# Kernel tuning notes

Measured on AMD Instinct MI355X. Metric: run time of the kernel, lower is better.

## Reference

```python
import jax, jax.numpy as jnp
import numpy as np

N, E = 50000, 800000
NF, EF, S = 128, 64, 128

def _lin(key, fan_in, fan_out):
    k1, k2 = jax.random.split(key)
    lim = 1.0 / np.sqrt(fan_in)
    W = jax.random.uniform(k1, (fan_in, fan_out), jnp.float32, -lim, lim)
    b = jax.random.uniform(k2, (fan_out,), jnp.float32, -lim, lim)
    return W, b

def setup_inputs() -> dict:
    key = jax.random.key(0)
    ks = jax.random.split(key, 12)
    x = jax.random.normal(ks[0], (N, NF), jnp.float32)
    edge_index = jax.random.randint(ks[1], (2, E), 0, N, jnp.int64)
    edge_attr = jax.random.normal(ks[2], (E, EF), jnp.float32)
    Wn, bn = _lin(ks[3], NF, S)
    We, be = _lin(ks[4], EF, S)
    Wzc, bzc = _lin(ks[5], S, S)   # GCNConv weight/bias (z gate)
    Wzl, bzl = _lin(ks[6], 2 * S, S)
    Wrc, brc = _lin(ks[7], S, S)
    Wrl, brl = _lin(ks[8], 2 * S, S)
    Whc, bhc = _lin(ks[9], S, S)
    Whl, bhl = _lin(ks[10], 2 * S, S)
    Wout, bout = _lin(ks[11], 3 * S, 1)
    return dict(x=x, edge_index=edge_index, edge_attr=edge_attr,
                Wn=Wn, bn=bn, We=We, be=be,
                Wzc=Wzc, bzc=bzc, Wzl=Wzl, bzl=bzl,
                Wrc=Wrc, brc=brc, Wrl=Wrl, brl=brl,
                Whc=Whc, bhc=bhc, Whl=Whl, bhl=bhl,
                Wout=Wout, bout=bout)

def reference(x, edge_index, edge_attr, Wn, bn, We, be,
              Wzc, bzc, Wzl, bzl, Wrc, brc, Wrl, brl,
              Whc, bhc, Whl, bhl, Wout, bout):
    n = x.shape[0]
    src, dst = edge_index[0], edge_index[1]
    xe = jax.nn.relu(x @ Wn + bn)                      # [N,S]
    ea = jax.nn.relu(edge_attr @ We + be)              # [E,S]
    # GCNConv normalization with self-loops (shared across the 3 gates)
    loop = jnp.arange(n)
    s2 = jnp.concatenate([src, loop])
    d2 = jnp.concatenate([dst, loop])
    deg = jax.ops.segment_sum(jnp.ones(s2.shape[0], xe.dtype), d2, n)
    dinv = jax.lax.rsqrt(deg)                          # deg >= 1 (self loops)
    norm = (dinv[s2] * dinv[d2])[:, None]              # [E+N,1]
    def gcn(W, b):
        xw = xe @ W
        return jax.ops.segment_sum(xw[s2] * norm, d2, n) + b
    H = jnp.zeros_like(xe)
    Z = jax.nn.sigmoid(jnp.concatenate([gcn(Wzc, bzc), H], 1) @ Wzl + bzl)
    R = jax.nn.sigmoid(jnp.concatenate([gcn(Wrc, brc), H], 1) @ Wrl + brl)
    Ht = jnp.tanh(jnp.concatenate([gcn(Whc, bhc), H * R], 1) @ Whl + bhl)
    H = Z * H + (1.0 - Z) * Ht                          # [N,S]
    edge_h = jnp.concatenate([H[src], H[dst], ea], axis=1)  # [E,3S]
    return edge_h @ Wout + bout                         # [E,1]
```

## Files before the change

kernel.cpp:

```cpp
#include <hip/hip_runtime.h>
#include <hip/hip_bf16.h>
#include <math.h>

#define NN 50000
#define EE 800000

typedef __bf16 bf16x8 __attribute__((ext_vector_type(8)));
typedef float f32x4 __attribute__((ext_vector_type(4)));
typedef unsigned int u32x4 __attribute__((ext_vector_type(4)));

__global__ void k_deg_wprep(const int* __restrict__ ei, int* __restrict__ deg,
                            const float* __restrict__ Wzc, const float* __restrict__ bzc,
                            const float* __restrict__ Wzl, const float* __restrict__ bzl,
                            const float* __restrict__ Whc, const float* __restrict__ bhc,
                            const float* __restrict__ Whl, const float* __restrict__ bhl,
                            float* __restrict__ Wcat, float* __restrict__ cb) {
    if (blockIdx.x < 128) {
        int i = blockIdx.x;
        int k = threadIdx.x;
        if (k < 128) {
            float sz = 0.f, sh = 0.f;
            for (int j = 0; j < 128; j++) {
                sz += Wzc[i * 128 + j] * Wzl[j * 128 + k];
                sh += Whc[i * 128 + j] * Whl[j * 128 + k];
            }
            Wcat[i * 256 + 2 * k]     = sz;
            Wcat[i * 256 + 2 * k + 1] = sh;
            if (i == 0) {
                float bz = bzl[k], bh = bhl[k];
                for (int j = 0; j < 128; j++) {
                    bz += bzc[j] * Wzl[j * 128 + k];
                    bh += bhc[j] * Whl[j * 128 + k];
                }
                cb[2 * k]     = bz;
                cb[2 * k + 1] = bh;
            }
        }
    } else {
        int e = (blockIdx.x - 128) * 256 + threadIdx.x;
        if (e < EE) atomicAdd(&deg[ei[EE + e]], 1);
    }
}

__global__ __launch_bounds__(256) void k_g1_mfma(const float* __restrict__ x,
                                                 const float* __restrict__ Wn,
                                                 const float* __restrict__ bn,
                                                 const int* __restrict__ deg,
                                                 __hip_bfloat16* __restrict__ xs) {
    const int lane = threadIdx.x & 63;
    const int ln = lane & 15;
    const int q  = lane >> 4;
    const int wid = (blockIdx.x * 256 + threadIdx.x) >> 6;
    const int nw  = gridDim.x * 4;
    const int ch  = wid & 1;
    const int step = nw >> 1;

    bf16x8 bfrag[4][4];
#pragma unroll
    for (int t = 0; t < 4; t++)
#pragma unroll
        for (int kc = 0; kc < 4; kc++)
#pragma unroll
            for (int j = 0; j < 8; j++)
                bfrag[t][kc][j] = (__bf16)Wn[(kc * 32 + q * 8 + j) * 128 + ch * 64 + t * 16 + ln];
    float biasR[4];
#pragma unroll
    for (int t = 0; t < 4; t++) biasR[t] = bn[ch * 64 + t * 16 + ln];

    for (int rt = wid >> 1; rt < 3125; rt += step) {
        const int e0 = rt * 16;
        const float* arow = x + (size_t)(e0 + ln) * 128;
        bf16x8 af[4];
#pragma unroll
        for (int kc = 0; kc < 4; kc++) {
            float4 v0 = *(const float4*)(arow + kc * 32 + q * 8);
            float4 v1 = *(const float4*)(arow + kc * 32 + q * 8 + 4);
            af[kc][0] = (__bf16)v0.x; af[kc][1] = (__bf16)v0.y;
            af[kc][2] = (__bf16)v0.z; af[kc][3] = (__bf16)v0.w;
            af[kc][4] = (__bf16)v1.x; af[kc][5] = (__bf16)v1.y;
            af[kc][6] = (__bf16)v1.z; af[kc][7] = (__bf16)v1.w;
        }
        f32x4 acc[4];
#pragma unroll
        for (int t = 0; t < 4; t++) acc[t] = (f32x4){0.f, 0.f, 0.f, 0.f};
#pragma unroll
        for (int t = 0; t < 4; t++)
#pragma unroll
            for (int kc = 0; kc < 4; kc++)
                acc[t] = __builtin_amdgcn_mfma_f32_16x16x32_bf16(af[kc], bfrag[t][kc], acc[t], 0, 0, 0);

        float diR[4];
#pragma unroll
        for (int r = 0; r < 4; r++) diR[r] = rsqrtf((float)(deg[e0 + q * 4 + r] + 1));
#pragma unroll
        for (int t = 0; t < 4; t++)
#pragma unroll
            for (int r = 0; r < 4; r++) {
                float v = fmaxf(acc[t][r] + biasR[t], 0.f) * diR[r];
                xs[(size_t)(e0 + q * 4 + r) * 128 + ch * 64 + t * 16 + ln] = __float2bfloat16(v);
            }
    }
}

__global__ void k_scan_a(const int* __restrict__ deg, int* __restrict__ partial) {
    __shared__ int s[256];
    int i = blockIdx.x * 256 + threadIdx.x;
    s[threadIdx.x] = (i < NN) ? deg[i] : 0;
    __syncthreads();
    for (int off = 128; off > 0; off >>= 1) {
        if (threadIdx.x < off) s[threadIdx.x] += s[threadIdx.x + off];
        __syncthreads();
    }
    if (threadIdx.x == 0) partial[blockIdx.x] = s[0];
}

__global__ void k_scan_c(const int* __restrict__ deg, const int* __restrict__ partial,
                         int* __restrict__ rowptr, int* __restrict__ cursor) {
    __shared__ int s[256];
    __shared__ int ps[256];
    int i = blockIdx.x * 256 + threadIdx.x;
    int v = (i < NN) ? deg[i] : 0;
    s[threadIdx.x] = v;
    ps[threadIdx.x] = (threadIdx.x < blockIdx.x) ? partial[threadIdx.x] : 0;
    __syncthreads();
    for (int off = 128; off > 0; off >>= 1) {
        if (threadIdx.x < off) ps[threadIdx.x] += ps[threadIdx.x + off];
        __syncthreads();
    }
    for (int off = 1; off < 256; off <<= 1) {
        int t = (threadIdx.x >= off) ? s[threadIdx.x - off] : 0;
        __syncthreads();
        s[threadIdx.x] += t;
        __syncthreads();
    }
    int excl = s[threadIdx.x] - v + ps[0];
    if (i < NN) { rowptr[i] = excl; cursor[i] = excl; }
    if (i == 0) rowptr[NN] = EE;
}

__global__ void k_fill(const int* __restrict__ ei, int* __restrict__ cursor,
                       int* __restrict__ col) {
    int e = blockIdx.x * 256 + threadIdx.x;
    if (e < EE) {
        int d = ei[EE + e];
        int p = atomicAdd(&cursor[d], 1);
        col[p] = ei[e];
    }
}

__global__ __launch_bounds__(256) void k_gather(const unsigned int* __restrict__ xsu,
                                                const int* __restrict__ rowptr,
                                                const int* __restrict__ col,
                                                const int* __restrict__ deg,
                                                unsigned int* __restrict__ aggu) {
    int gt = blockIdx.x * 256 + threadIdx.x;
    int node = gt >> 6;
    int lane = threadIdx.x & 63;
    if (node >= NN) return;
    const int g = lane >> 4;
    const int k = lane & 15;
    int beg = rowptr[node], end = rowptr[node + 1];

    float acc[8];
#pragma unroll
    for (int i = 0; i < 8; i++) acc[i] = 0.f;

    {
        u32x4 sv = *(const u32x4*)(xsu + (size_t)node * 64 + k * 4);
        if (g == 0) {
#pragma unroll
            for (int d = 0; d < 4; d++) {
                acc[2 * d]     += __uint_as_float(sv[d] << 16);
                acc[2 * d + 1] += __uint_as_float(sv[d] & 0xFFFF0000u);
            }
        }
    }

    int p = beg;
    while (p < end) {
        int rem = end - p;
        int chunk = rem < 64 ? rem : 64;
        int cv = (lane < chunk) ? col[p + lane] : 0;
        for (int j = 0; j < chunk; j += 4) {
            int s = __shfl(cv, j + g);
            u32x4 v = *(const u32x4*)(xsu + (size_t)s * 64 + k * 4);
            if (j + g >= chunk) v = (u32x4){0u, 0u, 0u, 0u};
#pragma unroll
            for (int d = 0; d < 4; d++) {
                acc[2 * d]     += __uint_as_float(v[d] << 16);
                acc[2 * d + 1] += __uint_as_float(v[d] & 0xFFFF0000u);
            }
        }
        p += 64;
    }

#pragma unroll
    for (int off = 16; off < 64; off <<= 1)
#pragma unroll
        for (int i = 0; i < 8; i++) acc[i] += __shfl_xor(acc[i], off);

    float di = rsqrtf((float)(deg[node] + 1));
    unsigned int o0, o1, o2, o3;
    {
        __hip_bfloat16 lo, hi;
        lo = __float2bfloat16(acc[0] * di); hi = __float2bfloat16(acc[1] * di);
        o0 = (unsigned int)*(unsigned short*)&lo | ((unsigned int)*(unsigned short*)&hi << 16);
        lo = __float2bfloat16(acc[2] * di); hi = __float2bfloat16(acc[3] * di);
        o1 = (unsigned int)*(unsigned short*)&lo | ((unsigned int)*(unsigned short*)&hi << 16);
        lo = __float2bfloat16(acc[4] * di); hi = __float2bfloat16(acc[5] * di);
        o2 = (unsigned int)*(unsigned short*)&lo | ((unsigned int)*(unsigned short*)&hi << 16);
        lo = __float2bfloat16(acc[6] * di); hi = __float2bfloat16(acc[7] * di);
        o3 = (unsigned int)*(unsigned short*)&lo | ((unsigned int)*(unsigned short*)&hi << 16);
    }
    int src = lane >> 2;
    unsigned int t0 = __shfl((int)o0, src);
    unsigned int t1 = __shfl((int)o1, src);
    unsigned int t2 = __shfl((int)o2, src);
    unsigned int t3 = __shfl((int)o3, src);
    int c2 = lane & 3;
    unsigned int res = (c2 == 0) ? t0 : (c2 == 1) ? t1 : (c2 == 2) ? t2 : t3;
    aggu[(size_t)node * 64 + lane] = res;
}

__global__ __launch_bounds__(256) void k_gate_red(const unsigned int* __restrict__ aggu,
                                                  const float* __restrict__ Wcat,
                                                  const float* __restrict__ cb,
                                                  const float* __restrict__ Wout,
                                                  float* __restrict__ aArr,
                                                  float* __restrict__ bArr) {
    __shared__ float red[4][32];
    const int lane = threadIdx.x & 63;
    const int ln = lane & 15;
    const int q  = lane >> 4;
    const int w  = threadIdx.x >> 6;

    bf16x8 bfrag[4][4];
#pragma unroll
    for (int t = 0; t < 4; t++)
#pragma unroll
        for (int kc = 0; kc < 4; kc++)
#pragma unroll
            for (int j = 0; j < 8; j++)
                bfrag[t][kc][j] = (__bf16)Wcat[(kc * 32 + q * 8 + j) * 256 + w * 64 + t * 16 + ln];

    float cbR[4], wAR[4], wBR[4];
#pragma unroll
    for (int t = 0; t < 4; t++) {
        int c = w * 64 + t * 16 + ln;
        cbR[t] = cb[c];
        int k = c >> 1;
        wAR[t] = Wout[k];
        wBR[t] = Wout[128 + k];
    }
    const bool odd = (ln & 1);

    for (int rt = blockIdx.x; rt < 3125; rt += gridDim.x) {
        const int e0 = rt * 16;
        const u32x4* arow = (const u32x4*)aggu + (size_t)(e0 + ln) * 16;
        bf16x8 af[4];
#pragma unroll
        for (int kc = 0; kc < 4; kc++) {
            u32x4 uv = arow[kc * 4 + q];
            af[kc] = __builtin_bit_cast(bf16x8, uv);
        }
        f32x4 acc[4];
#pragma unroll
        for (int t = 0; t < 4; t++) acc[t] = (f32x4){0.f, 0.f, 0.f, 0.f};
#pragma unroll
        for (int t = 0; t < 4; t++)
#pragma unroll
            for (int kc = 0; kc < 4; kc++)
                acc[t] = __builtin_amdgcn_mfma_f32_16x16x32_bf16(af[kc], bfrag[t][kc], acc[t], 0, 0, 0);

        float pa[4] = {0.f, 0.f, 0.f, 0.f};
        float pb[4] = {0.f, 0.f, 0.f, 0.f};
#pragma unroll
        for (int t = 0; t < 4; t++)
#pragma unroll
            for (int r = 0; r < 4; r++) {
                float val = acc[t][r] + cbR[t];
                float s = odd ? tanhf(val) : (1.f / (1.f + expf(-val)));
                float partner = __shfl_xor(s, 1);
                if (!odd) {
                    float h = (1.f - s) * partner;
                    pa[r] += h * wAR[t];
                    pb[r] += h * wBR[t];
                }
            }
#pragma unroll
        for (int off = 1; off < 16; off <<= 1) {
#pragma unroll
            for (int r = 0; r < 4; r++) {
                pa[r] += __shfl_xor(pa[r], off);
                pb[r] += __shfl_xor(pb[r], off);
            }
        }
        if (ln < 4) {
            float v = (ln == 0) ? pa[0] : (ln == 1) ? pa[1] : (ln == 2) ? pa[2] : pa[3];
            red[w][q * 4 + ln] = v;
        } else if (ln < 8) {
            int r = ln - 4;
            float v = (r == 0) ? pb[0] : (r == 1) ? pb[1] : (r == 2) ? pb[2] : pb[3];
            red[w][16 + q * 4 + r] = v;
        }
        __syncthreads();
        if (threadIdx.x < 32) {
            int row = threadIdx.x & 15;
            int ab = threadIdx.x >> 4;
            float s = red[0][ab * 16 + row] + red[1][ab * 16 + row]
                    + red[2][ab * 16 + row] + red[3][ab * 16 + row];
            if (ab) bArr[e0 + row] = s; else aArr[e0 + row] = s;
        }
        __syncthreads();
    }
}

__global__ __launch_bounds__(256) void k_edge_mfma(const float* __restrict__ EA,
                                                   const int* __restrict__ ei,
                                                   const float* __restrict__ We,
                                                   const float* __restrict__ be,
                                                   const float* __restrict__ Wout,
                                                   const float* __restrict__ boutp,
                                                   const float* __restrict__ aArr,
                                                   const float* __restrict__ bArr,
                                                   float* __restrict__ out) {
    const int lane = threadIdx.x & 63;
    const int ln = lane & 15;
    const int q  = lane >> 4;
    const int wid = (blockIdx.x * 256 + threadIdx.x) >> 6;
    const int nw  = gridDim.x * 4;

    bf16x8 bfrag[2][8];
#pragma unroll
    for (int h = 0; h < 2; h++)
#pragma unroll
        for (int t = 0; t < 8; t++)
#pragma unroll
            for (int j = 0; j < 8; j++)
                bfrag[h][t][j] = (__bf16)We[(h * 32 + q * 8 + j) * 128 + t * 16 + ln];

    float beR[8], w3R[8];
#pragma unroll
    for (int t = 0; t < 8; t++) {
        beR[t] = be[t * 16 + ln];
        w3R[t] = Wout[256 + t * 16 + ln];
    }
    const float b0 = boutp[0];

    for (int tile = wid; tile < EE / 16; tile += nw) {
        const int e0 = tile * 16;
        const float* arow = EA + (size_t)(e0 + ln) * 64;
        float4 v0 = *(const float4*)(arow + q * 8);
        float4 v1 = *(const float4*)(arow + q * 8 + 4);
        float4 v2 = *(const float4*)(arow + 32 + q * 8);
        float4 v3 = *(const float4*)(arow + 32 + q * 8 + 4);
        bf16x8 af0, af1;
        af0[0] = (__bf16)v0.x; af0[1] = (__bf16)v0.y; af0[2] = (__bf16)v0.z; af0[3] = (__bf16)v0.w;
        af0[4] = (__bf16)v1.x; af0[5] = (__bf16)v1.y; af0[6] = (__bf16)v1.z; af0[7] = (__bf16)v1.w;
        af1[0] = (__bf16)v2.x; af1[1] = (__bf16)v2.y; af1[2] = (__bf16)v2.z; af1[3] = (__bf16)v2.w;
        af1[4] = (__bf16)v3.x; af1[5] = (__bf16)v3.y; af1[6] = (__bf16)v3.z; af1[7] = (__bf16)v3.w;

        f32x4 acc[8];
#pragma unroll
        for (int t = 0; t < 8; t++) acc[t] = (f32x4){0.f, 0.f, 0.f, 0.f};
#pragma unroll
        for (int t = 0; t < 8; t++)
            acc[t] = __builtin_amdgcn_mfma_f32_16x16x32_bf16(af0, bfrag[0][t], acc[t], 0, 0, 0);
#pragma unroll
        for (int t = 0; t < 8; t++)
            acc[t] = __builtin_amdgcn_mfma_f32_16x16x32_bf16(af1, bfrag[1][t], acc[t], 0, 0, 0);

        float part[4] = {0.f, 0.f, 0.f, 0.f};
#pragma unroll
        for (int t = 0; t < 8; t++)
#pragma unroll
            for (int r = 0; r < 4; r++) {
                float y = acc[t][r] + beR[t];
                y = fmaxf(y, 0.f);
                part[r] += y * w3R[t];
            }
#pragma unroll
        for (int off = 1; off < 16; off <<= 1) {
#pragma unroll
            for (int r = 0; r < 4; r++) part[r] += __shfl_xor(part[r], off);
        }
        if (ln < 4) {
            float c = (ln == 0) ? part[0] : (ln == 1) ? part[1] : (ln == 2) ? part[2] : part[3];
            int e = e0 + q * 4 + ln;
            out[e] = c + aArr[ei[e]] + bArr[ei[EE + e]] + b0;
        }
    }
}

extern "C" void kernel_launch(void* const* d_in, const int* in_sizes, int n_in,
                              void* d_out, int out_size, void* d_ws, size_t ws_size,
                              hipStream_t stream) {
    const float* x    = (const float*)d_in[0];
    const int*   ei   = (const int*)d_in[1];
    const float* ea   = (const float*)d_in[2];
    const float* Wn   = (const float*)d_in[3];
    const float* bn   = (const float*)d_in[4];
    const float* We   = (const float*)d_in[5];
    const float* be   = (const float*)d_in[6];
    const float* Wzc  = (const float*)d_in[7];
    const float* bzc  = (const float*)d_in[8];
    const float* Wzl  = (const float*)d_in[9];
    const float* bzl  = (const float*)d_in[10];
    const float* Whc  = (const float*)d_in[15];
    const float* bhc  = (const float*)d_in[16];
    const float* Whl  = (const float*)d_in[17];
    const float* bhl  = (const float*)d_in[18];
    const float* Wout = (const float*)d_in[19];
    const float* bout = (const float*)d_in[20];
    float* out = (float*)d_out;

    char* w = (char*)d_ws;
    auto carve = [&](size_t bytes) {
        void* p = (void*)w;
        w += (bytes + 255) / 256 * 256;
        return p;
    };
    int*   deg     = (int*)carve((size_t)NN * 4);
    float* aArr    = (float*)carve((size_t)NN * 4);
    float* bArr    = (float*)carve((size_t)NN * 4);
    __hip_bfloat16* xs = (__hip_bfloat16*)carve((size_t)NN * 128 * 2);
    unsigned int* aggu = (unsigned int*)carve((size_t)NN * 64 * 4);
    float* Wcat    = (float*)carve(128 * 256 * 4);
    float* cb      = (float*)carve(256 * 4);
    int*   rowptr  = (int*)carve((size_t)(NN + 1) * 4);
    int*   cursor  = (int*)carve((size_t)NN * 4);
    int*   col     = (int*)carve((size_t)EE * 4);
    int*   partial = (int*)carve(256 * 4);

    hipMemsetAsync(deg, 0, (size_t)NN * 4, stream);

    k_deg_wprep<<<128 + 3125, 256, 0, stream>>>(ei, deg, Wzc, bzc, Wzl, bzl,
                                                Whc, bhc, Whl, bhl, Wcat, cb);

    k_g1_mfma<<<384, 256, 0, stream>>>(x, Wn, bn, deg, xs);

    const int NB = (NN + 255) / 256;
    k_scan_a<<<NB, 256, 0, stream>>>(deg, partial);
    k_scan_c<<<NB, 256, 0, stream>>>(deg, partial, rowptr, cursor);
    k_fill<<<3125, 256, 0, stream>>>(ei, cursor, col);

    k_gather<<<(NN * 64 + 255) / 256, 256, 0, stream>>>((const unsigned int*)xs, rowptr, col, deg, aggu);

    k_gate_red<<<512, 256, 0, stream>>>(aggu, Wcat, cb, Wout, aArr, bArr);

    k_edge_mfma<<<2048, 256, 0, stream>>>(ea, ei, We, be, Wout, bout, aArr, bArr, out);
}
```

Measured before the change: 530.0 us.

## Fuse node GEMM into degree kernel and apply source dinv during gather

The node-embedding MFMA GEMM no longer depends on degrees, so it moves into the same launch as the degree-count and weight-prep kernel, with its grid doubled to 768 blocks. The source-side normalization is now applied in the gather by loading a precomputed dinv per neighbor, and dinv is computed once in the scan kernel. This removes one kernel launch and the serial dependency, letting the dense GEMM overlap with the atomic degree counting. In exchange, the gather does an extra scalar load per neighbor and an extra multiply per element.

Result: faster. 514.5 us, median of 2 (-2.9%).

```diff
diff --git a/kernel.cpp b/kernel.cpp
--- a/kernel.cpp
+++ b/kernel.cpp
@@ -9,12 +9,15 @@
 typedef float f32x4 __attribute__((ext_vector_type(4)));
 typedef unsigned int u32x4 __attribute__((ext_vector_type(4)));
 
-__global__ void k_deg_wprep(const int* __restrict__ ei, int* __restrict__ deg,
+#define G1B 3253
+__global__ __launch_bounds__(256) void k_fused0(const int* __restrict__ ei, int* __restrict__ deg,
                             const float* __restrict__ Wzc, const float* __restrict__ bzc,
                             const float* __restrict__ Wzl, const float* __restrict__ bzl,
                             const float* __restrict__ Whc, const float* __restrict__ bhc,
                             const float* __restrict__ Whl, const float* __restrict__ bhl,
-                            float* __restrict__ Wcat, float* __restrict__ cb) {
+                            float* __restrict__ Wcat, float* __restrict__ cb,
+                            const float* __restrict__ x, const float* __restrict__ Wn,
+                            const float* __restrict__ bn, __hip_bfloat16* __restrict__ xs) {
     if (blockIdx.x < 128) {
         int i = blockIdx.x;
         int k = threadIdx.x;
@@ -36,69 +39,59 @@
                 cb[2 * k + 1] = bh;
             }
         }
-    } else {
+    } else if (blockIdx.x < G1B) {
         int e = (blockIdx.x - 128) * 256 + threadIdx.x;
         if (e < EE) atomicAdd(&deg[ei[EE + e]], 1);
-    }
-}
-
-__global__ __launch_bounds__(256) void k_g1_mfma(const float* __restrict__ x,
-                                                 const float* __restrict__ Wn,
-                                                 const float* __restrict__ bn,
-                                                 const int* __restrict__ deg,
-                                                 __hip_bfloat16* __restrict__ xs) {
-    const int lane = threadIdx.x & 63;
-    const int ln = lane & 15;
-    const int q  = lane >> 4;
-    const int wid = (blockIdx.x * 256 + threadIdx.x) >> 6;
-    const int nw  = gridDim.x * 4;
-    const int ch  = wid & 1;
-    const int step = nw >> 1;
-
-    bf16x8 bfrag[4][4];
-#pragma unroll
-    for (int t = 0; t < 4; t++)
-#pragma unroll
-        for (int kc = 0; kc < 4; kc++)
-#pragma unroll
-            for (int j = 0; j < 8; j++)
-                bfrag[t][kc][j] = (__bf16)Wn[(kc * 32 + q * 8 + j) * 128 + ch * 64 + t * 16 + ln];
-    float biasR[4];
-#pragma unroll
-    for (int t = 0; t < 4; t++) biasR[t] = bn[ch * 64 + t * 16 + ln];
-
-    for (int rt = wid >> 1; rt < 3125; rt += step) {
-        const int e0 = rt * 16;
-        const float* arow = x + (size_t)(e0 + ln) * 128;
-        bf16x8 af[4];
-#pragma unroll
-        for (int kc = 0; kc < 4; kc++) {
-            float4 v0 = *(const float4*)(arow + kc * 32 + q * 8);
-            float4 v1 = *(const float4*)(arow + kc * 32 + q * 8 + 4);
-            af[kc][0] = (__bf16)v0.x; af[kc][1] = (__bf16)v0.y;
-            af[kc][2] = (__bf16)v0.z; af[kc][3] = (__bf16)v0.w;
-            af[kc][4] = (__bf16)v1.x; af[kc][5] = (__bf16)v1.y;
-            af[kc][6] = (__bf16)v1.z; af[kc][7] = (__bf16)v1.w;
-        }
-        f32x4 acc[4];
-#pragma unroll
-        for (int t = 0; t < 4; t++) acc[t] = (f32x4){0.f, 0.f, 0.f, 0.f};
+    } else {
+        const int lane = threadIdx.x & 63;
+        const int ln = lane & 15;
+        const int q  = lane >> 4;
+        const int wid = ((blockIdx.x - G1B) * 256 + threadIdx.x) >> 6;
+        const int nw  = (gridDim.x - G1B) * 4;
+        const int ch  = wid & 1;
+        const int step = nw >> 1;
+
+        bf16x8 bfrag[4][4];
 #pragma unroll
         for (int t = 0; t < 4; t++)
 #pragma unroll
             for (int kc = 0; kc < 4; kc++)
-                acc[t] = __builtin_amdgcn_mfma_f32_16x16x32_bf16(af[kc], bfrag[t][kc], acc[t], 0, 0, 0);
-
-        float diR[4];
-#pragma unroll
-        for (int r = 0; r < 4; r++) diR[r] = rsqrtf((float)(deg[e0 + q * 4 + r] + 1));
-#pragma unroll
-        for (int t = 0; t < 4; t++)
-#pragma unroll
-            for (int r = 0; r < 4; r++) {
-                float v = fmaxf(acc[t][r] + biasR[t], 0.f) * diR[r];
-                xs[(size_t)(e0 + q * 4 + r) * 128 + ch * 64 + t * 16 + ln] = __float2bfloat16(v);
-            }
+#pragma unroll
+                for (int j = 0; j < 8; j++)
+                    bfrag[t][kc][j] = (__bf16)Wn[(kc * 32 + q * 8 + j) * 128 + ch * 64 + t * 16 + ln];
+        float biasR[4];
+#pragma unroll
+        for (int t = 0; t < 4; t++) biasR[t] = bn[ch * 64 + t * 16 + ln];
+
+        for (int rt = wid >> 1; rt < 3125; rt += step) {
+            const int e0 = rt * 16;
+            const float* arow = x + (size_t)(e0 + ln) * 128;
+            bf16x8 af[4];
+#pragma unroll
+            for (int kc = 0; kc < 4; kc++) {
+                float4 v0 = *(const float4*)(arow + kc * 32 + q * 8);
+                float4 v1 = *(const float4*)(arow + kc * 32 + q * 8 + 4);
+                af[kc][0] = (__bf16)v0.x; af[kc][1] = (__bf16)v0.y;
+                af[kc][2] = (__bf16)v0.z; af[kc][3] = (__bf16)v0.w;
+                af[kc][4] = (__bf16)v1.x; af[kc][5] = (__bf16)v1.y;
+                af[kc][6] = (__bf16)v1.z; af[kc][7] = (__bf16)v1.w;
+            }
+            f32x4 acc[4];
+#pragma unroll
+            for (int t = 0; t < 4; t++) acc[t] = (f32x4){0.f, 0.f, 0.f, 0.f};
+#pragma unroll
+            for (int t = 0; t < 4; t++)
+#pragma unroll
+                for (int kc = 0; kc < 4; kc++)
+                    acc[t] = __builtin_amdgcn_mfma_f32_16x16x32_bf16(af[kc], bfrag[t][kc], acc[t], 0, 0, 0);
+#pragma unroll
+            for (int t = 0; t < 4; t++)
+#pragma unroll
+                for (int r = 0; r < 4; r++) {
+                    float v = fmaxf(acc[t][r] + biasR[t], 0.f);
+                    xs[(size_t)(e0 + q * 4 + r) * 128 + ch * 64 + t * 16 + ln] = __float2bfloat16(v);
+                }
+        }
     }
 }
 
@@ -115,7 +108,8 @@
 }
 
 __global__ void k_scan_c(const int* __restrict__ deg, const int* __restrict__ partial,
-                         int* __restrict__ rowptr, int* __restrict__ cursor) {
+                         int* __restrict__ rowptr, int* __restrict__ cursor,
+                         float* __restrict__ dinvArr) {
     __shared__ int s[256];
     __shared__ int ps[256];
     int i = blockIdx.x * 256 + threadIdx.x;
@@ -134,7 +128,10 @@
         __syncthreads();
     }
     int excl = s[threadIdx.x] - v + ps[0];
-    if (i < NN) { rowptr[i] = excl; cursor[i] = excl; }
+    if (i < NN) {
+        rowptr[i] = excl; cursor[i] = excl;
+        dinvArr[i] = rsqrtf((float)(v + 1));
+    }
     if (i == 0) rowptr[NN] = EE;
 }
 
@@ -151,7 +148,7 @@
 __global__ __launch_bounds__(256) void k_gather(const unsigned int* __restrict__ xsu,
                                                 const int* __restrict__ rowptr,
                                                 const int* __restrict__ col,
-                                                const int* __restrict__ deg,
+                                                const float* __restrict__ dinvArr,
                                                 unsigned int* __restrict__ aggu) {
     int gt = blockIdx.x * 256 + threadIdx.x;
     int node = gt >> 6;
@@ -160,6 +157,7 @@
     const int g = lane >> 4;
     const int k = lane & 15;
     int beg = rowptr[node], end = rowptr[node + 1];
+    const float dn = dinvArr[node];
 
     float acc[8];
 #pragma unroll
@@ -170,8 +168,8 @@
         if (g == 0) {
 #pragma unroll
             for (int d = 0; d < 4; d++) {
-                acc[2 * d]     += __uint_as_float(sv[d] << 16);
-                acc[2 * d + 1] += __uint_as_float(sv[d] & 0xFFFF0000u);
+                acc[2 * d]     += dn * __uint_as_float(sv[d] << 16);
+                acc[2 * d + 1] += dn * __uint_as_float(sv[d] & 0xFFFF0000u);
             }
         }
     }
@@ -183,12 +181,13 @@
         int cv = (lane < chunk) ? col[p + lane] : 0;
         for (int j = 0; j < chunk; j += 4) {
             int s = __shfl(cv, j + g);
+            float dv = dinvArr[s];
             u32x4 v = *(const u32x4*)(xsu + (size_t)s * 64 + k * 4);
             if (j + g >= chunk) v = (u32x4){0u, 0u, 0u, 0u};
 #pragma unroll
             for (int d = 0; d < 4; d++) {
-                acc[2 * d]     += __uint_as_float(v[d] << 16);
-                acc[2 * d + 1] += __uint_as_float(v[d] & 0xFFFF0000u);
+                acc[2 * d]     += dv * __uint_as_float(v[d] << 16);
+                acc[2 * d + 1] += dv * __uint_as_float(v[d] & 0xFFFF0000u);
             }
         }
         p += 64;
@@ -199,17 +198,16 @@
 #pragma unroll
         for (int i = 0; i < 8; i++) acc[i] += __shfl_xor(acc[i], off);
 
-    float di = rsqrtf((float)(deg[node] + 1));
     unsigned int o0, o1, o2, o3;
     {
         __hip_bfloat16 lo, hi;
-        lo = __float2bfloat16(acc[0] * di); hi = __float2bfloat16(acc[1] * di);
+        lo = __float2bfloat16(acc[0] * dn); hi = __float2bfloat16(acc[1] * dn);
         o0 = (unsigned int)*(unsigned short*)&lo | ((unsigned int)*(unsigned short*)&hi << 16);
-        lo = __float2bfloat16(acc[2] * di); hi = __float2bfloat16(acc[3] * di);
+        lo = __float2bfloat16(acc[2] * dn); hi = __float2bfloat16(acc[3] * dn);
         o1 = (unsigned int)*(unsigned short*)&lo | ((unsigned int)*(unsigned short*)&hi << 16);
-        lo = __float2bfloat16(acc[4] * di); hi = __float2bfloat16(acc[5] * di);
+        lo = __float2bfloat16(acc[4] * dn); hi = __float2bfloat16(acc[5] * dn);
         o2 = (unsigned int)*(unsigned short*)&lo | ((unsigned int)*(unsigned short*)&hi << 16);
-        lo = __float2bfloat16(acc[6] * di); hi = __float2bfloat16(acc[7] * di);
+        lo = __float2bfloat16(acc[6] * dn); hi = __float2bfloat16(acc[7] * dn);
         o3 = (unsigned int)*(unsigned short*)&lo | ((unsigned int)*(unsigned short*)&hi << 16);
     }
     int src = lane >> 2;
@@ -423,6 +421,7 @@
     int*   deg     = (int*)carve((size_t)NN * 4);
     float* aArr    = (float*)carve((size_t)NN * 4);
     float* bArr    = (float*)carve((size_t)NN * 4);
+    float* dinvArr = (float*)carve((size_t)NN * 4);
     __hip_bfloat16* xs = (__hip_bfloat16*)carve((size_t)NN * 128 * 2);
     unsigned int* aggu = (unsigned int*)carve((size_t)NN * 64 * 4);
     float* Wcat    = (float*)carve(128 * 256 * 4);
@@ -434,17 +433,16 @@
 
     hipMemsetAsync(deg, 0, (size_t)NN * 4, stream);
 
-    k_deg_wprep<<<128 + 3125, 256, 0, stream>>>(ei, deg, Wzc, bzc, Wzl, bzl,
-                                                Whc, bhc, Whl, bhl, Wcat, cb);
-
-    k_g1_mfma<<<384, 256, 0, stream>>>(x, Wn, bn, deg, xs);
+    k_fused0<<<G1B + 768, 256, 0, stream>>>(ei, deg, Wzc, bzc, Wzl, bzl,
+                                            Whc, bhc, Whl, bhl, Wcat, cb,
+                                            x, Wn, bn, xs);
 
     const int NB = (NN + 255) / 256;
     k_scan_a<<<NB, 256, 0, stream>>>(deg, partial);
-    k_scan_c<<<NB, 256, 0, stream>>>(deg, partial, rowptr, cursor);
+    k_scan_c<<<NB, 256, 0, stream>>>(deg, partial, rowptr, cursor, dinvArr);
     k_fill<<<3125, 256, 0, stream>>>(ei, cursor, col);
 
-    k_gather<<<(NN * 64 + 255) / 256, 256, 0, stream>>>((const unsigned int*)xs, rowptr, col, deg, aggu);
+    k_gather<<<(NN * 64 + 255) / 256, 256, 0, stream>>>((const unsigned int*)xs, rowptr, col, dinvArr, aggu);
 
     k_gate_red<<<512, 256, 0, stream>>>(aggu, Wcat, cb, Wout, aArr, bArr);
 
```
